# Optimization experiments

Hardware: AMD Instinct MI355X
Metric: run time of the kernel (lower is better)

Reference implementation:

```python
import jax, jax.numpy as jnp
import numpy as np

SOFT_BLEND = 20.0
INIT_BONES = np.array([0, 1, 2, 4, 5, 16, 17, 18, 19])
MAX_STEPS = 20
CVG_THRESH = 1e-5
DVG_THRESH = 1.0
EPS = 1e-6


def mlp(x, W0, b0, W1, b1, W2, b2):
    h = jax.nn.softplus(x @ W0 + b0)
    h = jax.nn.softplus(h @ W1 + b1)
    return h @ W2 + b2


def query_weights(x, params):
    # lbs_network -> soft_blend * logits -> softmax  (softmax_mode='softmax')
    return jax.nn.softmax(SOFT_BLEND * mlp(x, *params), axis=-1)


def forward_skinning(xc, params, tfs):
    # xc [B,N,3], tfs [B,J,4,4] -> xd [B,N,3]  (LBS: blend transforms with weights)
    w = query_weights(xc, params)                                    # [B,N,J]
    xh = jnp.concatenate([xc, jnp.ones_like(xc[..., :1])], -1)       # [B,N,4]
    return jnp.einsum('bpn,bnij,bpj->bpi', w, tfs, xh)[..., :3]


def gradient(xc, params, tfs):
    # per-point jacobian d(forward_skinning)/d(xc): [B,N,3,3]
    def f(x, tfs_b):
        w = query_weights(x, params)                                 # [J]
        xh = jnp.concatenate([x, jnp.ones((1,), x.dtype)])
        return jnp.einsum('j,jik,k->i', w, tfs_b, xh)[:3]
    jac = jax.jacfwd(f)
    return jax.vmap(jax.vmap(jac, in_axes=(0, None)), in_axes=(0, 0))(xc, tfs)


def broyden(g, x_init, J_inv_init):
    # vectorized Broyden: the torch data-dependent boolean masking becomes
    # mask-gated jnp.where updates; the early break becomes a fixed-length scan
    # (iterations are no-ops once ids_val is all False).
    x = x_init                                                       # [M,3,1]
    J_inv = J_inv_init                                               # [M,3,3]
    gx = g(x)
    update = -(J_inv @ gx)
    gx_norm_opt = jnp.linalg.norm(gx[..., 0], axis=-1)               # [M]
    state = (x, gx, J_inv, update, gx_norm_opt,
             jnp.zeros_like(x), jnp.zeros_like(gx),
             jnp.ones_like(gx_norm_opt, dtype=bool))

    def step(s, _):
        x, gx, J_inv, update, gx_norm_opt, delta_x, delta_gx, ids_val = s
        m = ids_val[:, None, None]
        delta_x = jnp.where(m, update, delta_x)
        x = x + jnp.where(m, delta_x, 0.0)
        gx_new = g(x)
        delta_gx = jnp.where(m, gx_new - gx, delta_gx)
        gx = jnp.where(m, gx_new, gx)
        gx_norm = jnp.linalg.norm(gx[..., 0], axis=-1)
        ids_opt = gx_norm < gx_norm_opt
        gx_norm_opt = jnp.where(ids_opt, gx_norm, gx_norm_opt)
        ids_val = (gx_norm_opt > CVG_THRESH) & (gx_norm < DVG_THRESH)
        m2 = ids_val[:, None, None]
        vT = jnp.swapaxes(delta_x, -1, -2) @ J_inv                   # [M,1,3]
        a = delta_x - J_inv @ delta_gx                               # [M,3,1]
        b = vT @ delta_gx                                            # [M,1,1]
        b = b + jnp.where(b >= 0, EPS, -EPS)
        J_inv = J_inv + jnp.where(m2, (a / b) @ vT, 0.0)
        update = -(J_inv @ gx)
        return (x, gx, J_inv, update, gx_norm_opt, delta_x, delta_gx, ids_val), None

    state, _ = jax.lax.scan(step, state, None, length=MAX_STEPS)
    # in the torch code x_opt aliases x, so the returned root is the final x
    return state[0], state[4]


def _forward(xd, tfs, W0, b0, W1, b1, W2, b2):
    params = (W0, b0, W1, b1, W2, b2)
    sg = jax.lax.stop_gradient
    B, N, D = xd.shape
    I = len(INIT_BONES)
    # ---- init: inverse rigid transform per init bone (one-hot weights) ----
    xdh = jnp.concatenate([xd, jnp.ones_like(xd[..., :1])], -1)      # [B,N,4]
    T_inv = jnp.linalg.inv(tfs[:, INIT_BONES])                        # [B,I,4,4]
    xc_init = jnp.einsum('bcij,bnj->bnci', T_inv, xdh)[..., :3]       # [B,N,I,3]
    # ---- Broyden correspondence search (torch.no_grad) ----
    params_sg = tuple(sg(p) for p in params)
    tfs_sg = sg(tfs)
    xc_flat = sg(xc_init).reshape(B, N * I, D)
    xd_tgt = sg(jnp.repeat(xd, I, axis=1))                            # [B,N*I,3]
    J_inv_init = jnp.linalg.inv(gradient(xc_flat, params_sg, tfs_sg)).reshape(-1, D, D)

    def g(x):                                                         # [M,3,1] -> [M,3,1]
        xc = x[..., 0].reshape(B, N * I, D)
        err = forward_skinning(xc, params_sg, tfs_sg) - xd_tgt
        return err.reshape(-1, D, 1)

    x_opt, _ = broyden(g, xc_flat.reshape(-1, D, 1), J_inv_init)
    xc_opt = sg(x_opt[..., 0].reshape(B, N * I, D))
    # ---- implicit differentiation correction term ----
    xd_opt = forward_skinning(xc_opt, params, tfs)
    grad_inv = sg(jnp.linalg.inv(gradient(xc_opt, params, tfs)))      # [B,M,3,3]
    correction = xd_opt - sg(xd_opt)
    correction = jnp.einsum('bnij,bnj->bni', -grad_inv, correction)
    return (xc_opt + correction).reshape(B, N, I, D)


def setup_inputs():
    key = jax.random.key(0)
    ks = jax.random.split(key, 6)
    B, N, J, W = 1, 30000, 24, 64
    xd = 0.5 * jax.random.normal(ks[0], (B, N, 3), jnp.float32)
    # near-rigid bone transforms: identity + small perturbation, homogeneous last row
    R = jnp.eye(3, dtype=jnp.float32) + 0.1 * jax.random.normal(ks[1], (B, J, 3, 3), jnp.float32)
    t = 0.2 * jax.random.normal(ks[2], (B, J, 3, 1), jnp.float32)
    bot = jnp.broadcast_to(jnp.array([0., 0., 0., 1.], jnp.float32), (B, J, 1, 4))
    tfs = jnp.concatenate([jnp.concatenate([R, t], -1), bot], -2)     # [B,J,4,4]
    W0 = 0.5 * jax.random.normal(ks[3], (3, W), jnp.float32)
    W1 = jax.random.normal(ks[4], (W, W), jnp.float32) / float(np.sqrt(W))
    W2 = 0.1 * jax.random.normal(ks[5], (W, J), jnp.float32) / float(np.sqrt(W))
    return {"xd": xd, "tfs": tfs,
            "W0": W0, "b0": jnp.zeros((W,), jnp.float32),
            "W1": W1, "b1": jnp.zeros((W,), jnp.float32),
            "W2": W2, "b2": jnp.zeros((J,), jnp.float32)}


def reference(xd, tfs, W0, b0, W1, b1, W2, b2):
    return _forward(xd, tfs, W0, b0, W1, b1, W2, b2)
```

## Files before the change

kernel.cpp:

```cpp
#include <hip/hip_runtime.h>
#include <math.h>

#define TPB 64
#define NPT 270000
#define SOFTB 20.0f
#define CVGT 1e-5f
#define DVGT 1.0f
#define EPSB 1e-6f

#define WS_TINV 0
#define WS_W0T  256

__global__ void prep_kernel(const float* __restrict__ tfs,
                            const float* __restrict__ W0, const float* __restrict__ b0,
                            float* __restrict__ ws) {
    int t = threadIdx.x;
    if (t < 9) {
        const int bones[9] = {0, 1, 2, 4, 5, 16, 17, 18, 19};
        const float* T = tfs + bones[t] * 16;
        float r00=T[0], r01=T[1], r02=T[2],  t0=T[3];
        float r10=T[4], r11=T[5], r12=T[6],  t1=T[7];
        float r20=T[8], r21=T[9], r22=T[10], t2=T[11];
        float c00 = r11*r22 - r12*r21;
        float c01 = r12*r20 - r10*r22;
        float c02 = r10*r21 - r11*r20;
        float det = r00*c00 + r01*c01 + r02*c02;
        float id  = 1.0f / det;
        float i00=c00*id, i01=(r02*r21-r01*r22)*id, i02=(r01*r12-r02*r11)*id;
        float i10=c01*id, i11=(r00*r22-r02*r20)*id, i12=(r02*r10-r00*r12)*id;
        float i20=c02*id, i21=(r01*r20-r00*r21)*id, i22=(r00*r11-r01*r10)*id;
        float* O = ws + WS_TINV + t * 16;
        O[0]=i00; O[1]=i01; O[2]=i02;  O[3]=-(i00*t0+i01*t1+i02*t2);
        O[4]=i10; O[5]=i11; O[6]=i12;  O[7]=-(i10*t0+i11*t1+i12*t2);
        O[8]=i20; O[9]=i21; O[10]=i22; O[11]=-(i20*t0+i21*t1+i22*t2);
        O[12]=0.f; O[13]=0.f; O[14]=0.f; O[15]=1.f;
    }
    for (int i = t; i < 64*4; i += 256) {
        int k = i >> 2, cidx = i & 3;
        ws[WS_W0T + i] = (cidx < 3) ? W0[cidx*64 + k] : b0[k];
    }
}

__global__ __launch_bounds__(TPB) void deform_kernel(
    const float* __restrict__ xd,
    const float* __restrict__ tfs,
    const float* __restrict__ W1, const float* __restrict__ b1,
    const float* __restrict__ W2, const float* __restrict__ b2,
    const float* __restrict__ ws,
    float* __restrict__ out)
{
    const int tid = threadIdx.x;
    const int p   = blockIdx.x * TPB + tid;
    const bool live = (p < NPT);
    const int pc = live ? p : 0;
    const int n  = pc / 9;
    const int c  = pc - n * 9;

    const float tx0 = xd[n*3+0], tx1 = xd[n*3+1], tx2 = xd[n*3+2];

    const float* Ti  = ws + WS_TINV + c * 16;
    const float* W0T = ws + WS_W0T;

    float x0 = fmaf(Ti[0], tx0, fmaf(Ti[1], tx1, fmaf(Ti[2],  tx2, Ti[3])));
    float x1 = fmaf(Ti[4], tx0, fmaf(Ti[5], tx1, fmaf(Ti[6],  tx2, Ti[7])));
    float x2 = fmaf(Ti[8], tx0, fmaf(Ti[9], tx1, fmaf(Ti[10], tx2, Ti[11])));

    float wreg[24];

    auto forward = [&](float a0, float a1, float a2, float& o0, float& o1, float& o2) {
        #pragma unroll
        for (int q = 0; q < 24; ++q) wreg[q] = b2[q];
        #pragma unroll 1
        for (int cc = 0; cc < 2; ++cc) {
            float z1c[32];
            const float* b1c = b1 + cc*32;
            #pragma unroll
            for (int j = 0; j < 32; ++j) z1c[j] = b1c[j];
            #pragma unroll 2
            for (int k = 0; k < 64; ++k) {
                float w0a = W0T[k*4+0], w0b = W0T[k*4+1], w0c = W0T[k*4+2], w0d = W0T[k*4+3];
                float z  = fmaf(a0, w0a, fmaf(a1, w0b, fmaf(a2, w0c, w0d)));
                float hk = fmaxf(z, 0.f) + __logf(1.f + __expf(-fabsf(z)));
                const float* Wr = W1 + k*64 + cc*32;
                #pragma unroll
                for (int j = 0; j < 32; ++j) z1c[j] = fmaf(hk, Wr[j], z1c[j]);
            }
            #pragma unroll
            for (int j = 0; j < 32; ++j) {
                float zz = z1c[j];
                float h  = fmaxf(zz, 0.f) + __logf(1.f + __expf(-fabsf(zz)));
                const float* W2r = W2 + (cc*32 + j)*24;
                #pragma unroll
                for (int q = 0; q < 24; ++q) wreg[q] = fmaf(h, W2r[q], wreg[q]);
            }
        }
        float t0 = fmaxf(wreg[0],  wreg[1]),  t1 = fmaxf(wreg[2],  wreg[3]);
        float t2 = fmaxf(wreg[4],  wreg[5]),  t3 = fmaxf(wreg[6],  wreg[7]);
        float t4 = fmaxf(wreg[8],  wreg[9]),  t5 = fmaxf(wreg[10], wreg[11]);
        float t6 = fmaxf(wreg[12], wreg[13]), t7 = fmaxf(wreg[14], wreg[15]);
        float t8 = fmaxf(wreg[16], wreg[17]), t9 = fmaxf(wreg[18], wreg[19]);
        float ta = fmaxf(wreg[20], wreg[21]), tb = fmaxf(wreg[22], wreg[23]);
        t0 = fmaxf(t0, t1); t2 = fmaxf(t2, t3); t4 = fmaxf(t4, t5);
        t6 = fmaxf(t6, t7); t8 = fmaxf(t8, t9); ta = fmaxf(ta, tb);
        t0 = fmaxf(t0, t2); t4 = fmaxf(t4, t6); t8 = fmaxf(t8, ta);
        float mx = fmaxf(fmaxf(t0, t4), t8);
        float ssum = 0.f;
        #pragma unroll
        for (int q = 0; q < 24; ++q) { float e = __expf(SOFTB*(wreg[q]-mx)); wreg[q] = e; ssum += e; }
        float inv = 1.0f / ssum;
        o0 = 0.f; o1 = 0.f; o2 = 0.f;
        #pragma unroll
        for (int q = 0; q < 24; ++q) {
            float wq = wreg[q] * inv;
            wreg[q] = wq;
            const float* Tn = tfs + q*16;
            float y0 = fmaf(Tn[0], a0, fmaf(Tn[1], a1, fmaf(Tn[2],  a2, Tn[3])));
            float y1 = fmaf(Tn[4], a0, fmaf(Tn[5], a1, fmaf(Tn[6],  a2, Tn[7])));
            float y2 = fmaf(Tn[8], a0, fmaf(Tn[9], a1, fmaf(Tn[10], a2, Tn[11])));
            o0 = fmaf(wq, y0, o0); o1 = fmaf(wq, y1, o1); o2 = fmaf(wq, y2, o2);
        }
    };

    float f0, f1, f2;
    forward(x0, x1, x2, f0, f1, f2);

    float Jm[9];
    #pragma unroll 1
    for (int t = 0; t < 3; ++t) {
        float dot = 0.f, sA = 0.f, sB = 0.f, sC = 0.f;
        #pragma unroll 1
        for (int cc = 0; cc < 4; ++cc) {
            float z1c[16], d1c[16];
            const float* b1c = b1 + cc*16;
            #pragma unroll
            for (int j = 0; j < 16; ++j) { z1c[j] = b1c[j]; d1c[j] = 0.f; }
            #pragma unroll 2
            for (int k = 0; k < 64; ++k) {
                float w0a = W0T[k*4+0], w0b = W0T[k*4+1], w0c = W0T[k*4+2], w0d = W0T[k*4+3];
                float wt  = W0T[k*4 + t];
                float z  = fmaf(x0, w0a, fmaf(x1, w0b, fmaf(x2, w0c, w0d)));
                float e  = __expf(-z);
                float hk = z + __logf(1.f + e);
                float sg = 1.0f / (1.0f + e);
                float dh0 = sg * wt;
                const float* Wr = W1 + k*64 + cc*16;
                #pragma unroll
                for (int j = 0; j < 16; ++j) {
                    z1c[j] = fmaf(hk,  Wr[j], z1c[j]);
                    d1c[j] = fmaf(dh0, Wr[j], d1c[j]);
                }
            }
            float dmc[24];
            #pragma unroll
            for (int q = 0; q < 24; ++q) dmc[q] = 0.f;
            #pragma unroll
            for (int j = 0; j < 16; ++j) {
                float sg1 = 1.0f / (1.0f + __expf(-z1c[j]));
                float dh1 = d1c[j] * sg1;
                const float* W2r = W2 + (cc*16 + j)*24;
                #pragma unroll
                for (int q = 0; q < 24; ++q) dmc[q] = fmaf(dh1, W2r[q], dmc[q]);
            }
            #pragma unroll
            for (int q = 0; q < 24; ++q) {
                float wd = wreg[q] * dmc[q];
                dot += wd;
                const float* Tn = tfs + q*16;
                float y0 = fmaf(Tn[0], x0, fmaf(Tn[1], x1, fmaf(Tn[2],  x2, Tn[3])));
                float y1 = fmaf(Tn[4], x0, fmaf(Tn[5], x1, fmaf(Tn[6],  x2, Tn[7])));
                float y2 = fmaf(Tn[8], x0, fmaf(Tn[9], x1, fmaf(Tn[10], x2, Tn[11])));
                sA = fmaf(wd, y0, sA); sB = fmaf(wd, y1, sB); sC = fmaf(wd, y2, sC);
            }
        }
        float ab0 = 0.f, ab1 = 0.f, ab2 = 0.f;
        #pragma unroll
        for (int q = 0; q < 24; ++q) {
            float wq = wreg[q];
            const float* Tn = tfs + q*16;
            ab0 = fmaf(wq, Tn[0 + t], ab0);
            ab1 = fmaf(wq, Tn[4 + t], ab1);
            ab2 = fmaf(wq, Tn[8 + t], ab2);
        }
        Jm[0 + t] = ab0 + SOFTB*(sA - dot*f0);
        Jm[3 + t] = ab1 + SOFTB*(sB - dot*f1);
        Jm[6 + t] = ab2 + SOFTB*(sC - dot*f2);
    }

    float m00=Jm[0], m01=Jm[1], m02=Jm[2];
    float m10=Jm[3], m11=Jm[4], m12=Jm[5];
    float m20=Jm[6], m21=Jm[7], m22=Jm[8];
    float c00 = m11*m22 - m12*m21, c01 = m12*m20 - m10*m22, c02 = m10*m21 - m11*m20;
    float det = m00*c00 + m01*c01 + m02*c02;
    float idet = 1.0f / det;
    float Ji0=c00*idet, Ji1=(m02*m21-m01*m22)*idet, Ji2=(m01*m12-m02*m11)*idet;
    float Ji3=c01*idet, Ji4=(m00*m22-m02*m20)*idet, Ji5=(m02*m10-m00*m12)*idet;
    float Ji6=c02*idet, Ji7=(m01*m20-m00*m21)*idet, Ji8=(m00*m11-m01*m10)*idet;

    float g0 = f0 - tx0, g1 = f1 - tx1, g2 = f2 - tx2;
    float gno = sqrtf(g0*g0 + g1*g1 + g2*g2);
    float u0 = -(Ji0*g0 + Ji1*g1 + Ji2*g2);
    float u1 = -(Ji3*g0 + Ji4*g1 + Ji5*g2);
    float u2 = -(Ji6*g0 + Ji7*g1 + Ji8*g2);
    bool valid = true;

    for (int it = 0; it < 20; ++it) {
        if (!__any((int)valid)) break;
        if (valid) {
            float dx0 = u0, dx1 = u1, dx2 = u2;
            x0 += dx0; x1 += dx1; x2 += dx2;
            float fn0, fn1, fn2;
            forward(x0, x1, x2, fn0, fn1, fn2);
            float ng0 = fn0 - tx0, ng1 = fn1 - tx1, ng2 = fn2 - tx2;
            float dg0 = ng0 - g0, dg1 = ng1 - g1, dg2 = ng2 - g2;
            g0 = ng0; g1 = ng1; g2 = ng2;
            float gn = sqrtf(g0*g0 + g1*g1 + g2*g2);
            gno = fminf(gn, gno);
            valid = (gno > CVGT) && (gn < DVGT);
            if (valid) {
                float v0 = dx0*Ji0 + dx1*Ji3 + dx2*Ji6;
                float v1 = dx0*Ji1 + dx1*Ji4 + dx2*Ji7;
                float v2 = dx0*Ji2 + dx1*Ji5 + dx2*Ji8;
                float a0 = dx0 - (Ji0*dg0 + Ji1*dg1 + Ji2*dg2);
                float a1 = dx1 - (Ji3*dg0 + Ji4*dg1 + Ji5*dg2);
                float a2 = dx2 - (Ji6*dg0 + Ji7*dg1 + Ji8*dg2);
                float b = v0*dg0 + v1*dg1 + v2*dg2;
                b += (b >= 0.f) ? EPSB : -EPSB;
                float ib = 1.0f / b;
                a0 *= ib; a1 *= ib; a2 *= ib;
                Ji0 = fmaf(a0, v0, Ji0); Ji1 = fmaf(a0, v1, Ji1); Ji2 = fmaf(a0, v2, Ji2);
                Ji3 = fmaf(a1, v0, Ji3); Ji4 = fmaf(a1, v1, Ji4); Ji5 = fmaf(a1, v2, Ji5);
                Ji6 = fmaf(a2, v0, Ji6); Ji7 = fmaf(a2, v1, Ji7); Ji8 = fmaf(a2, v2, Ji8);
                u0 = -(Ji0*g0 + Ji1*g1 + Ji2*g2);
                u1 = -(Ji3*g0 + Ji4*g1 + Ji5*g2);
                u2 = -(Ji6*g0 + Ji7*g1 + Ji8*g2);
            }
        }
    }

    if (live) {
        out[p*3+0] = x0;
        out[p*3+1] = x1;
        out[p*3+2] = x2;
    }
}

extern "C" void kernel_launch(void* const* d_in, const int* in_sizes, int n_in,
                              void* d_out, int out_size, void* d_ws, size_t ws_size,
                              hipStream_t stream) {
    const float* xd  = (const float*)d_in[0];
    const float* tfs = (const float*)d_in[1];
    const float* W0  = (const float*)d_in[2];
    const float* b0  = (const float*)d_in[3];
    const float* W1  = (const float*)d_in[4];
    const float* b1  = (const float*)d_in[5];
    const float* W2  = (const float*)d_in[6];
    const float* b2  = (const float*)d_in[7];
    float* out = (float*)d_out;
    float* ws  = (float*)d_ws;

    prep_kernel<<<1, 256, 0, stream>>>(tfs, W0, b0, ws);
    int nblk = (NPT + TPB - 1) / TPB;
    deform_kernel<<<nblk, TPB, 0, stream>>>(xd, tfs, W1, b1, W2, b2, ws, out);
}
```

Measured before the change: 836.0 us.

## Compact active Broyden lanes across block each iteration to reduce warp divergence

Raises the block from one wavefront to four and, at every Broyden iteration, stream-compacts the still-active points into the lowest thread slots via shared memory (ballot/popcount prefix plus a 23-float state spill). Points write their output as soon as they converge or diverge, so whole wavefronts become idle and can skip the expensive MLP forward instead of running it masked. The cost is two block barriers and a round trip of about 23 floats of state through LDS per iteration, plus about 23 KB of shared memory per block, which may limit occupancy.

New measurement: 823.5 us. No clear change (-1.5%).

```diff
diff --git a/kernel.cpp b/kernel.cpp
--- a/kernel.cpp
+++ b/kernel.cpp
@@ -1,7 +1,8 @@
 #include <hip/hip_runtime.h>
 #include <math.h>
 
-#define TPB 64
+#define BLK 256
+#define NW  4
 #define NPT 270000
 #define SOFTB 20.0f
 #define CVGT 1e-5f
@@ -41,7 +42,7 @@
     }
 }
 
-__global__ __launch_bounds__(TPB) void deform_kernel(
+__global__ __launch_bounds__(BLK) void deform_kernel(
     const float* __restrict__ xd,
     const float* __restrict__ tfs,
     const float* __restrict__ W1, const float* __restrict__ b1,
@@ -49,14 +50,17 @@
     const float* __restrict__ ws,
     float* __restrict__ out)
 {
+    __shared__ float st[23 * BLK];
+    __shared__ int scnt[NW];
+
     const int tid = threadIdx.x;
-    const int p   = blockIdx.x * TPB + tid;
-    const bool live = (p < NPT);
-    const int pc = live ? p : 0;
+    int p = blockIdx.x * BLK + tid;
+    bool active = (p < NPT);
+    const int pc = active ? p : 0;
     const int n  = pc / 9;
     const int c  = pc - n * 9;
 
-    const float tx0 = xd[n*3+0], tx1 = xd[n*3+1], tx2 = xd[n*3+2];
+    float tx0 = xd[n*3+0], tx1 = xd[n*3+1], tx2 = xd[n*3+2];
 
     const float* Ti  = ws + WS_TINV + c * 16;
     const float* W0T = ws + WS_W0T;
@@ -201,11 +205,43 @@
     float u0 = -(Ji0*g0 + Ji1*g1 + Ji2*g2);
     float u1 = -(Ji3*g0 + Ji4*g1 + Ji5*g2);
     float u2 = -(Ji6*g0 + Ji7*g1 + Ji8*g2);
-    bool valid = true;
-
+
+    const int lane = tid & 63, wid = tid >> 6;
     for (int it = 0; it < 20; ++it) {
-        if (!__any((int)valid)) break;
-        if (valid) {
+        unsigned long long mask = __ballot((int)active);
+        if (lane == 0) scnt[wid] = __popcll(mask);
+        __syncthreads();
+        int nact = scnt[0] + scnt[1] + scnt[2] + scnt[3];
+        if (nact == 0) break;
+        int off = 0;
+        if (wid > 0) off += scnt[0];
+        if (wid > 1) off += scnt[1];
+        if (wid > 2) off += scnt[2];
+        int slot = off + __popcll(mask & ((1ull << lane) - 1));
+        if (active) {
+            st[ 0*BLK+slot]=x0;  st[ 1*BLK+slot]=x1;  st[ 2*BLK+slot]=x2;
+            st[ 3*BLK+slot]=tx0; st[ 4*BLK+slot]=tx1; st[ 5*BLK+slot]=tx2;
+            st[ 6*BLK+slot]=g0;  st[ 7*BLK+slot]=g1;  st[ 8*BLK+slot]=g2;
+            st[ 9*BLK+slot]=u0;  st[10*BLK+slot]=u1;  st[11*BLK+slot]=u2;
+            st[12*BLK+slot]=Ji0; st[13*BLK+slot]=Ji1; st[14*BLK+slot]=Ji2;
+            st[15*BLK+slot]=Ji3; st[16*BLK+slot]=Ji4; st[17*BLK+slot]=Ji5;
+            st[18*BLK+slot]=Ji6; st[19*BLK+slot]=Ji7; st[20*BLK+slot]=Ji8;
+            st[21*BLK+slot]=gno;
+            st[22*BLK+slot]=__int_as_float(p);
+        }
+        __syncthreads();
+        active = (tid < nact);
+        if (active) {
+            x0 =st[ 0*BLK+tid]; x1 =st[ 1*BLK+tid]; x2 =st[ 2*BLK+tid];
+            tx0=st[ 3*BLK+tid]; tx1=st[ 4*BLK+tid]; tx2=st[ 5*BLK+tid];
+            g0 =st[ 6*BLK+tid]; g1 =st[ 7*BLK+tid]; g2 =st[ 8*BLK+tid];
+            u0 =st[ 9*BLK+tid]; u1 =st[10*BLK+tid]; u2 =st[11*BLK+tid];
+            Ji0=st[12*BLK+tid]; Ji1=st[13*BLK+tid]; Ji2=st[14*BLK+tid];
+            Ji3=st[15*BLK+tid]; Ji4=st[16*BLK+tid]; Ji5=st[17*BLK+tid];
+            Ji6=st[18*BLK+tid]; Ji7=st[19*BLK+tid]; Ji8=st[20*BLK+tid];
+            gno=st[21*BLK+tid];
+            p  =__float_as_int(st[22*BLK+tid]);
+
             float dx0 = u0, dx1 = u1, dx2 = u2;
             x0 += dx0; x1 += dx1; x2 += dx2;
             float fn0, fn1, fn2;
@@ -215,7 +251,7 @@
             g0 = ng0; g1 = ng1; g2 = ng2;
             float gn = sqrtf(g0*g0 + g1*g1 + g2*g2);
             gno = fminf(gn, gno);
-            valid = (gno > CVGT) && (gn < DVGT);
+            bool valid = (gno > CVGT) && (gn < DVGT);
             if (valid) {
                 float v0 = dx0*Ji0 + dx1*Ji3 + dx2*Ji6;
                 float v1 = dx0*Ji1 + dx1*Ji4 + dx2*Ji7;
@@ -233,11 +269,14 @@
                 u0 = -(Ji0*g0 + Ji1*g1 + Ji2*g2);
                 u1 = -(Ji3*g0 + Ji4*g1 + Ji5*g2);
                 u2 = -(Ji6*g0 + Ji7*g1 + Ji8*g2);
-            }
-        }
-    }
-
-    if (live) {
+            } else {
+                out[p*3+0] = x0; out[p*3+1] = x1; out[p*3+2] = x2;
+                active = false;
+            }
+        }
+    }
+
+    if (active) {
         out[p*3+0] = x0;
         out[p*3+1] = x1;
         out[p*3+2] = x2;
@@ -259,6 +298,6 @@
     float* ws  = (float*)d_ws;
 
     prep_kernel<<<1, 256, 0, stream>>>(tfs, W0, b0, ws);
-    int nblk = (NPT + TPB - 1) / TPB;
-    deform_kernel<<<nblk, TPB, 0, stream>>>(xd, tfs, W1, b1, W2, b2, ws, out);
+    int nblk = (NPT + BLK - 1) / BLK;
+    deform_kernel<<<nblk, BLK, 0, stream>>>(xd, tfs, W1, b1, W2, b2, ws, out);
 }
```
